# Kernel tuning notes

Hardware: AMD Instinct MI355X
Metric: run time of the kernel (lower is better)

The kernel has to match this reference:

```python
import jax, jax.numpy as jnp
import numpy as np

N = 10000      # nodes
E = 320000     # edges (before self-loops)
D_IN = 256
HID = 128
HEADS = 4
D_OUT = 256
SLOPE = 0.2    # PyG GATConv default negative_slope


def setup_inputs() -> dict:
    key = jax.random.key(0)
    ks = jax.random.split(key, 10)
    s = 0.05
    return {
        "x": jax.random.normal(ks[0], (N, D_IN), dtype=jnp.float32),
        "edge_index": jax.random.randint(ks[1], (2, E), 0, N),
        # layer 1: in=256 -> heads=4, out=128, concat
        "W1": jax.random.normal(ks[2], (D_IN, HEADS * HID), dtype=jnp.float32) * s,
        "a1_src": jax.random.normal(ks[3], (HEADS, HID), dtype=jnp.float32) * s,
        "a1_dst": jax.random.normal(ks[4], (HEADS, HID), dtype=jnp.float32) * s,
        "b1": jax.random.normal(ks[5], (HEADS * HID,), dtype=jnp.float32) * s,
        # layer 2: in=512 -> heads=1, out=256, no concat
        "W2": jax.random.normal(ks[6], (HEADS * HID, D_OUT), dtype=jnp.float32) * s,
        "a2_src": jax.random.normal(ks[7], (1, D_OUT), dtype=jnp.float32) * s,
        "a2_dst": jax.random.normal(ks[8], (1, D_OUT), dtype=jnp.float32) * s,
        "b2": jax.random.normal(ks[9], (D_OUT,), dtype=jnp.float32) * s,
    }


def gat_conv(x, src, dst, W, a_src, a_dst, bias, heads, out_dim, concat):
    """PyG-style GATConv (eval mode, self-loops pre-added to src/dst)."""
    n = x.shape[0]
    h = (x @ W).reshape(n, heads, out_dim)            # [N, H, F]
    # per-edge attention logits: LeakyReLU(a_src.h_src + a_dst.h_dst)
    as_n = (h * a_src).sum(-1)                         # [N, H]
    ad_n = (h * a_dst).sum(-1)                         # [N, H]
    logit = jax.nn.leaky_relu(as_n[src] + ad_n[dst], negative_slope=SLOPE)  # [E, H]
    # segment softmax over edges grouped by destination node
    logit = logit - jax.ops.segment_max(logit, dst, num_segments=n)[dst]
    ex = jnp.exp(logit)
    alpha = ex / jax.ops.segment_sum(ex, dst, num_segments=n)[dst]          # [E, H]
    # weighted scatter-aggregation of source messages
    out = jax.ops.segment_sum(h[src] * alpha[:, :, None], dst, num_segments=n)  # [N, H, F]
    out = out.reshape(n, heads * out_dim) if concat else out.mean(axis=1)
    return out + bias


def reference(x, edge_index, W1, a1_src, a1_dst, b1, W2, a2_src, a2_dst, b2):
    # add self-loops once (PyG GATConv default add_self_loops=True)
    loops = jnp.arange(N, dtype=edge_index.dtype)
    src = jnp.concatenate([edge_index[0], loops])
    dst = jnp.concatenate([edge_index[1], loops])
    h = gat_conv(x, src, dst, W1, a1_src, a1_dst, b1, HEADS, HID, True)
    h = jax.nn.elu(h)  # dropout is identity at eval
    return gat_conv(h, src, dst, W2, a2_src, a2_dst, b2, 1, D_OUT, False)
```

## Files before the change

kernel.cpp:

```cpp
#include <hip/hip_runtime.h>

#define N_NODES 10000
#define E_RAW   320000
#define E_TOT   330000
#define D_IN    256
#define HID     128
#define HEADS   4
#define F1      512
#define D_OUT   256
#define SLOPE   0.2f
#define EBLOCKS 1290

typedef __attribute__((ext_vector_type(8))) short bf16x8;
typedef __attribute__((ext_vector_type(4))) float f32x4;

__device__ __forceinline__ float bf2f(ushort u) {
    return __uint_as_float(((uint)u) << 16);
}
__device__ __forceinline__ ushort f2bf(float x) {
    uint u = __float_as_uint(x);
    uint r = (u + 0x7FFFu + ((u >> 16) & 1u)) >> 16;
    return (ushort)r;
}
__device__ __forceinline__ float bfu_lo(uint u) { return __uint_as_float(u << 16); }
__device__ __forceinline__ float bfu_hi(uint u) { return __uint_as_float(u & 0xFFFF0000u); }

__device__ __forceinline__ void gload_lds16(const void* g, void* l) {
    __builtin_amdgcn_global_load_lds(
        (const __attribute__((address_space(1))) void*)g,
        (__attribute__((address_space(3))) void*)l, 16, 0, 0);
}


__global__ __launch_bounds__(256) void k_zero_all(int* __restrict__ deg,
                                                  float* __restrict__ as1,
                                                  float* __restrict__ ad1,
                                                  float* __restrict__ as2,
                                                  float* __restrict__ ad2) {
    int i = blockIdx.x * 256 + threadIdx.x;
    if (i < 4 * N_NODES) { as1[i] = 0.f; ad1[i] = 0.f; }
    if (i < N_NODES) { deg[i] = 0; as2[i] = 0.f; ad2[i] = 0.f; }
}


__global__ __launch_bounds__(256) void k_hist(const int* __restrict__ ei, int* __restrict__ deg) {
    int e = blockIdx.x * 256 + threadIdx.x;
    if (e < E_TOT) {
        int dst = (e < E_RAW) ? ei[E_RAW + e] : (e - E_RAW);
        atomicAdd(&deg[dst], 1);
    }
}


#define SCAN_CHUNK 40

__global__ __launch_bounds__(256) void k_prep(const int* __restrict__ deg,
                                              int* __restrict__ row_start,
                                              int* __restrict__ cursor,
                                              const float* __restrict__ W1,
                                              ushort* __restrict__ w1h,
                                              const float* __restrict__ W2,
                                              ushort* __restrict__ w2h,
                                              const float* __restrict__ x,
                                              ushort* __restrict__ xb) {
    int b = blockIdx.x;
    int tid = threadIdx.x;
    if (b == 0) {
        __shared__ int tots[256];
        int base = tid * SCAN_CHUNK;
        int loc[SCAN_CHUNK];
        int s = 0;
        #pragma unroll
        for (int k = 0; k < SCAN_CHUNK; k++) {
            int idx = base + k;
            int v = (idx < N_NODES) ? deg[idx] : 0;
            loc[k] = s;
            s += v;
        }
        tots[tid] = s;
        __syncthreads();
        for (int off = 1; off < 256; off <<= 1) {
            int t = (tid >= off) ? tots[tid - off] : 0;
            __syncthreads();
            tots[tid] += t;
            __syncthreads();
        }
        int excl = tots[tid] - s;
        #pragma unroll
        for (int k = 0; k < SCAN_CHUNK; k++) {
            int idx = base + k;
            if (idx < N_NODES) {
                int r = excl + loc[k];
                row_start[idx] = r;
                cursor[idx]    = r;
            }
        }
        if (tid == 255) row_start[N_NODES] = E_TOT;
    } else if (b <= 512) {
        int i = (b - 1) * 256 + tid;
        int k = i / F1, n = i - k * F1;
        w1h[(size_t)n * D_IN + k] = f2bf(W1[i]);
    } else if (b <= 1024) {
        int i = (b - 513) * 256 + tid;
        int k = i / D_OUT, n = i - k * D_OUT;
        w2h[(size_t)n * F1 + k] = f2bf(W2[i]);
    } else {
        int i8 = (b - 1025) * 256 + tid;
        float4 a = *(const float4*)&x[(size_t)i8 * 8];
        float4 c = *(const float4*)&x[(size_t)i8 * 8 + 4];
        uint4 u;
        u.x = (uint)f2bf(a.x) | ((uint)f2bf(a.y) << 16);
        u.y = (uint)f2bf(a.z) | ((uint)f2bf(a.w) << 16);
        u.z = (uint)f2bf(c.x) | ((uint)f2bf(c.y) << 16);
        u.w = (uint)f2bf(c.z) | ((uint)f2bf(c.w) << 16);
        *(uint4*)&xb[(size_t)i8 * 8] = u;
    }
}


template<int BM, int KD, int ND, int WC, int HMUL>
__device__ __forceinline__ void gemm_attn(int bx, int by, int tid,
                                          const ushort* __restrict__ A,
                                          const ushort* __restrict__ B,
                                          ushort* __restrict__ C,
                                          const float* __restrict__ avs,
                                          const float* __restrict__ avd,
                                          float* __restrict__ os,
                                          float* __restrict__ od) {
    constexpr int WR = 4 / WC;
    constexpr int MI = (BM / WR) / 16;
    constexpr int NJ = (64 / WC) / 16;
    __shared__ ushort sA[BM * 64];
    __shared__ ushort sB[64 * 64];

    const int lane = tid & 63;
    const int wid = tid >> 6;
    const int wr = wid / WC;
    const int wc = wid % WC;
    const int m0 = by * BM;
    const int n0 = bx * 64;
    const int fr = lane & 15;
    const int fs = lane >> 4;
    const int rowc = lane >> 3;
    const int slot = (lane & 7) ^ rowc;

    f32x4 acc[MI][NJ];
    #pragma unroll
    for (int i = 0; i < MI; i++)
        #pragma unroll
        for (int j = 0; j < NJ; j++) acc[i][j] = (f32x4){0.f, 0.f, 0.f, 0.f};

    for (int k0 = 0; k0 < KD; k0 += 64) {
        #pragma unroll
        for (int t = 0; t < BM / 32; t++) {
            int c = wid + 4 * t;
            int gr = m0 + c * 8 + rowc;
            gr = gr < N_NODES ? gr : N_NODES - 1;
            gload_lds16(A + (size_t)gr * KD + k0 + slot * 8, &sA[c * 512]);
        }
        #pragma unroll
        for (int t = 0; t < 2; t++) {
            int c = wid + 4 * t;
            gload_lds16(B + (size_t)(n0 + c * 8 + rowc) * KD + k0 + slot * 8, &sB[c * 512]);
        }
        __syncthreads();
        #pragma unroll
        for (int kk = 0; kk < 2; kk++) {
            int sbase = kk * 4 + fs;
            bf16x8 a_f[MI], b_f[NJ];
            #pragma unroll
            for (int i = 0; i < MI; i++) {
                int r = wr * 64 + i * 16 + fr;
                a_f[i] = *(const bf16x8*)&sA[r * 64 + ((sbase ^ (r & 7)) << 3)];
            }
            #pragma unroll
            for (int j = 0; j < NJ; j++) {
                int cc = wc * (64 / WC) + j * 16 + fr;
                b_f[j] = *(const bf16x8*)&sB[cc * 64 + ((sbase ^ (cc & 7)) << 3)];
            }
            #pragma unroll
            for (int i = 0; i < MI; i++)
                #pragma unroll
                for (int j = 0; j < NJ; j++)
                    acc[i][j] = __builtin_amdgcn_mfma_f32_16x16x32_bf16(a_f[i], b_f[j], acc[i][j], 0, 0, 0);
        }
        __syncthreads();
    }

    const int hoff = (HMUL == 4) ? (n0 >> 7) : 0;
    float sv[NJ], dv[NJ];
    int cols[NJ];
    #pragma unroll
    for (int j = 0; j < NJ; j++) {
        cols[j] = n0 + wc * (64 / WC) + j * 16 + fr;
        sv[j] = avs[cols[j]];
        dv[j] = avd[cols[j]];
    }
    #pragma unroll
    for (int i = 0; i < MI; i++) {
        int row_base = m0 + wr * 64 + i * 16 + (fs << 2);
        float ps[4], pd[4];
        #pragma unroll
        for (int q = 0; q < 4; q++) {
            int r = row_base + q;
            float p_s = 0.f, p_d = 0.f;
            #pragma unroll
            for (int j = 0; j < NJ; j++) {
                float v = acc[i][j][q];
                if (r < N_NODES) C[(size_t)r * ND + cols[j]] = f2bf(v);
                p_s += v * sv[j];
                p_d += v * dv[j];
            }
            ps[q] = p_s; pd[q] = p_d;
        }
        #pragma unroll
        for (int q = 0; q < 4; q++) {
            #pragma unroll
            for (int m = 8; m >= 1; m >>= 1) {
                ps[q] += __shfl_xor(ps[q], m, 16);
                pd[q] += __shfl_xor(pd[q], m, 16);
            }
        }
        if (fr == 0) {
            #pragma unroll
            for (int q = 0; q < 4; q++) {
                int r = row_base + q;
                if (r < N_NODES) {
                    atomicAdd(&os[r * HMUL + hoff], ps[q]);
                    atomicAdd(&od[r * HMUL + hoff], pd[q]);
                }
            }
        }
    }
}


__global__ __launch_bounds__(256) void k_mid(const int* __restrict__ ei,
                                             int* __restrict__ cursor,
                                             int* __restrict__ csr_src,
                                             const ushort* __restrict__ xb,
                                             const ushort* __restrict__ w1h,
                                             ushort* __restrict__ h1,
                                             const float* __restrict__ a1s,
                                             const float* __restrict__ a1d,
                                             float* __restrict__ as1,
                                             float* __restrict__ ad1) {
    int b = blockIdx.x;
    if (b < EBLOCKS) {
        int e = b * 256 + threadIdx.x;
        if (e < E_TOT) {
            int src = (e < E_RAW) ? ei[e] : (e - E_RAW);
            int dst = (e < E_RAW) ? ei[E_RAW + e] : (e - E_RAW);
            int pos = atomicAdd(&cursor[dst], 1);
            csr_src[pos] = src;
        }
        return;
    }
    int g = b - EBLOCKS;
    gemm_attn<128, D_IN, F1, 2, 4>(g % 8, g / 8, threadIdx.x,
                                   xb, w1h, h1, a1s, a1d, as1, ad1);
}


__global__ __launch_bounds__(256) void k_gemm2(const ushort* __restrict__ heluh,
                                               const ushort* __restrict__ w2h,
                                               ushort* __restrict__ h2,
                                               const float* __restrict__ a2s,
                                               const float* __restrict__ a2d,
                                               float* __restrict__ as2,
                                               float* __restrict__ ad2) {
    int b = blockIdx.x;
    gemm_attn<64, F1, D_OUT, 4, 1>(b % 4, b / 4, threadIdx.x,
                                   heluh, w2h, h2, a2s, a2d, as2, ad2);
}


__device__ __forceinline__ void fma8(uint4 v, float e, float* acc) {
    acc[0] += bfu_lo(v.x) * e; acc[1] += bfu_hi(v.x) * e;
    acc[2] += bfu_lo(v.y) * e; acc[3] += bfu_hi(v.y) * e;
    acc[4] += bfu_lo(v.z) * e; acc[5] += bfu_hi(v.z) * e;
    acc[6] += bfu_lo(v.w) * e; acc[7] += bfu_hi(v.w) * e;
}

__global__ __launch_bounds__(256) void k_edge1(const int* __restrict__ row_start,
                                               const int* __restrict__ csr_src,
                                               const ushort* __restrict__ h1,
                                               const float* __restrict__ as1,
                                               const float* __restrict__ ad1,
                                               const float* __restrict__ b1,
                                               ushort* __restrict__ heluh) {
    int node = blockIdx.x * 4 + (threadIdx.x >> 6);
    int lane = threadIdx.x & 63;
    int start = row_start[node];
    int end   = row_start[node + 1];
    int h_lane = lane >> 4;

    float adl = ad1[node * 4 + h_lane];

    float acc[8] = {0,0,0,0,0,0,0,0};
    float sum = 0.f;
    const size_t lo8 = (size_t)lane * 8;

    int i = start;
    for (; i + 8 <= end; i += 8) {
        int s[8];
        #pragma unroll
        for (int k = 0; k < 8; k++) s[k] = csr_src[i + k];
        float l[8];
        #pragma unroll
        for (int k = 0; k < 8; k++) l[k] = as1[s[k] * 4 + h_lane];
        uint4 v[8];
        #pragma unroll
        for (int k = 0; k < 8; k++) v[k] = *(const uint4*)(h1 + (size_t)s[k] * F1 + lo8);
        #pragma unroll
        for (int k = 0; k < 8; k++) {
            float t = l[k] + adl;
            t = t > 0.f ? t : SLOPE * t;
            float e = __expf(t);
            sum += e;
            fma8(v[k], e, acc);
        }
    }
    for (; i < end; i++) {
        int s0 = csr_src[i];
        float t = as1[s0 * 4 + h_lane] + adl;
        uint4 v0 = *(const uint4*)(h1 + (size_t)s0 * F1 + lo8);
        t = t > 0.f ? t : SLOPE * t;
        float e = __expf(t);
        sum += e;
        fma8(v0, e, acc);
    }
    float inv = 1.f / sum;

    size_t o = (size_t)node * F1 + lo8;
    const float* bp = b1 + lo8;
    uint pk[4];
    #pragma unroll
    for (int j = 0; j < 4; j++) {
        float v0 = acc[2*j]   * inv + bp[2*j];
        float v1 = acc[2*j+1] * inv + bp[2*j+1];
        v0 = v0 > 0.f ? v0 : (__expf(v0) - 1.f);
        v1 = v1 > 0.f ? v1 : (__expf(v1) - 1.f);
        pk[j] = (uint)f2bf(v0) | ((uint)f2bf(v1) << 16);
    }
    *(uint4*)&heluh[o] = make_uint4(pk[0], pk[1], pk[2], pk[3]);
}

__global__ __launch_bounds__(256) void k_edge2(const int* __restrict__ row_start,
                                               const int* __restrict__ csr_src,
                                               const ushort* __restrict__ h2,
                                               const float* __restrict__ as2,
                                               const float* __restrict__ ad2,
                                               const float* __restrict__ b2,
                                               float* __restrict__ out) {
    int node = blockIdx.x * 4 + (threadIdx.x >> 6);
    int lane = threadIdx.x & 63;
    int sub = lane >> 5;
    int fl  = lane & 31;
    int start = row_start[node];
    int end   = row_start[node + 1];

    float ad = ad2[node];

    float acc[8] = {0,0,0,0,0,0,0,0};
    float sum = 0.f;
    const size_t fo = (size_t)fl * 8;

    int i = start;
    for (; i + 8 <= end; i += 8) {
        int s[4];
        #pragma unroll
        for (int k = 0; k < 4; k++) s[k] = csr_src[i + 2 * k + sub];
        float l[4];
        #pragma unroll
        for (int k = 0; k < 4; k++) l[k] = as2[s[k]];
        uint4 v[4];
        #pragma unroll
        for (int k = 0; k < 4; k++) v[k] = *(const uint4*)(h2 + (size_t)s[k] * D_OUT + fo);
        #pragma unroll
        for (int k = 0; k < 4; k++) {
            float t = l[k] + ad;
            t = t > 0.f ? t : SLOPE * t;
            float e = __expf(t);
            sum += e;
            fma8(v[k], e, acc);
        }
    }
    for (; i < end; i += 2) {
        if (i + sub < end) {
            int s0 = csr_src[i + sub];
            float t = as2[s0] + ad;
            uint4 v0 = *(const uint4*)(h2 + (size_t)s0 * D_OUT + fo);
            t = t > 0.f ? t : SLOPE * t;
            float e = __expf(t);
            sum += e;
            fma8(v0, e, acc);
        }
    }
    #pragma unroll
    for (int j = 0; j < 8; j++) acc[j] += __shfl_xor(acc[j], 32, 64);
    sum += __shfl_xor(sum, 32, 64);
    float inv = 1.f / sum;

    if (lane < 32) {
        size_t o = (size_t)node * D_OUT + fo;
        const float* bp = b2 + fo;
        float4 r0, r1;
        r0.x = acc[0] * inv + bp[0]; r0.y = acc[1] * inv + bp[1];
        r0.z = acc[2] * inv + bp[2]; r0.w = acc[3] * inv + bp[3];
        r1.x = acc[4] * inv + bp[4]; r1.y = acc[5] * inv + bp[5];
        r1.z = acc[6] * inv + bp[6]; r1.w = acc[7] * inv + bp[7];
        *(float4*)&out[o] = r0;
        *(float4*)&out[o + 4] = r1;
    }
}


extern "C" void kernel_launch(void* const* d_in, const int* in_sizes, int n_in,
                              void* d_out, int out_size, void* d_ws, size_t ws_size,
                              hipStream_t stream) {
    const float* x   = (const float*)d_in[0];
    const int*   ei  = (const int*)d_in[1];
    const float* W1  = (const float*)d_in[2];
    const float* a1s = (const float*)d_in[3];
    const float* a1d = (const float*)d_in[4];
    const float* b1  = (const float*)d_in[5];
    const float* W2  = (const float*)d_in[6];
    const float* a2s = (const float*)d_in[7];
    const float* a2d = (const float*)d_in[8];
    const float* b2  = (const float*)d_in[9];
    float* out = (float*)d_out;

    char* ws = (char*)d_ws;
    size_t off = 0;
    auto take = [&](size_t bytes) {
        char* p = ws + off;
        off += (bytes + 255) & ~(size_t)255;
        return p;
    };
    int*    deg       = (int*)take(sizeof(int) * N_NODES);
    int*    row_start = (int*)take(sizeof(int) * (N_NODES + 1));
    int*    cursor    = (int*)take(sizeof(int) * N_NODES);
    int*    csr_src   = (int*)take(sizeof(int) * E_TOT);
    ushort* xb        = (ushort*)take(sizeof(ushort) * (size_t)N_NODES * D_IN);
    ushort* w1h       = (ushort*)take(sizeof(ushort) * D_IN * F1);
    ushort* w2h       = (ushort*)take(sizeof(ushort) * F1 * D_OUT);
    ushort* h1        = (ushort*)take(sizeof(ushort) * (size_t)N_NODES * F1);
    float*  as1       = (float*)take(sizeof(float) * N_NODES * 4);
    float*  ad1       = (float*)take(sizeof(float) * N_NODES * 4);
    ushort* heluh     = (ushort*)take(sizeof(ushort) * (size_t)N_NODES * F1);
    ushort* h2        = (ushort*)take(sizeof(ushort) * (size_t)N_NODES * D_OUT);
    float*  as2       = (float*)take(sizeof(float) * N_NODES);
    float*  ad2       = (float*)take(sizeof(float) * N_NODES);

    k_zero_all<<<(4 * N_NODES + 255) / 256, 256, 0, stream>>>(deg, as1, ad1, as2, ad2);
    k_hist<<<EBLOCKS, 256, 0, stream>>>(ei, deg);
    k_prep<<<2275, 256, 0, stream>>>(deg, row_start, cursor, W1, w1h, W2, w2h, x, xb);
    k_mid<<<EBLOCKS + 8 * 79, 256, 0, stream>>>(ei, cursor, csr_src, xb, w1h, h1,
                                                a1s, a1d, as1, ad1);
    k_edge1<<<N_NODES / 4, 256, 0, stream>>>(row_start, csr_src, h1, as1, ad1, b1, heluh);
    k_gemm2<<<4 * 157, 256, 0, stream>>>(heluh, w2h, h2, a2s, a2d, as2, ad2);
    k_edge2<<<N_NODES / 4, 256, 0, stream>>>(row_start, csr_src, h2, as2, ad2, b2, out);
}
```

Measured before the change: 169.9 us.

## Double-buffer GEMM LDS tiles, vectorize weight transposes, split scatter from GEMM1

The GEMM tile loop now double-buffers its shared-memory A/B tiles, so the next K-slice load is issued before computing the current one and one barrier per iteration is dropped. The weight transpose-to-bf16 step now has each thread gather 8 K values and write them as one 16-byte store, which cuts block count and the scattered 2-byte writes. The edge CSR scatter is split out of the combined k_mid launch into its own kernel, and GEMM1 gets a dedicated kernel. This adds one kernel launch and doubles LDS use per block, which may lower occupancy.

```diff
diff --git a/kernel.cpp b/kernel.cpp
--- a/kernel.cpp
+++ b/kernel.cpp
@@ -96,16 +96,36 @@
             }
         }
         if (tid == 255) row_start[N_NODES] = E_TOT;
-    } else if (b <= 512) {
-        int i = (b - 1) * 256 + tid;
-        int k = i / F1, n = i - k * F1;
-        w1h[(size_t)n * D_IN + k] = f2bf(W1[i]);
-    } else if (b <= 1024) {
-        int i = (b - 513) * 256 + tid;
-        int k = i / D_OUT, n = i - k * D_OUT;
-        w2h[(size_t)n * F1 + k] = f2bf(W2[i]);
+    } else if (b <= 64) {
+        int task = (b - 1) * 4 + (tid >> 6);
+        int lane = tid & 63;
+        int n = (task >> 5) * 64 + lane;
+        int k0 = (task & 31) * 8;
+        float v[8];
+        #pragma unroll
+        for (int j = 0; j < 8; j++) v[j] = W1[(size_t)(k0 + j) * F1 + n];
+        uint4 u;
+        u.x = (uint)f2bf(v[0]) | ((uint)f2bf(v[1]) << 16);
+        u.y = (uint)f2bf(v[2]) | ((uint)f2bf(v[3]) << 16);
+        u.z = (uint)f2bf(v[4]) | ((uint)f2bf(v[5]) << 16);
+        u.w = (uint)f2bf(v[6]) | ((uint)f2bf(v[7]) << 16);
+        *(uint4*)&w1h[(size_t)n * D_IN + k0] = u;
+    } else if (b <= 128) {
+        int task = (b - 65) * 4 + (tid >> 6);
+        int lane = tid & 63;
+        int n = (task >> 6) * 64 + lane;
+        int k0 = (task & 63) * 8;
+        float v[8];
+        #pragma unroll
+        for (int j = 0; j < 8; j++) v[j] = W2[(size_t)(k0 + j) * D_OUT + n];
+        uint4 u;
+        u.x = (uint)f2bf(v[0]) | ((uint)f2bf(v[1]) << 16);
+        u.y = (uint)f2bf(v[2]) | ((uint)f2bf(v[3]) << 16);
+        u.z = (uint)f2bf(v[4]) | ((uint)f2bf(v[5]) << 16);
+        u.w = (uint)f2bf(v[6]) | ((uint)f2bf(v[7]) << 16);
+        *(uint4*)&w2h[(size_t)n * F1 + k0] = u;
     } else {
-        int i8 = (b - 1025) * 256 + tid;
+        int i8 = (b - 129) * 256 + tid;
         float4 a = *(const float4*)&x[(size_t)i8 * 8];
         float4 c = *(const float4*)&x[(size_t)i8 * 8 + 4];
         uint4 u;
@@ -114,6 +134,19 @@
         u.z = (uint)f2bf(c.x) | ((uint)f2bf(c.y) << 16);
         u.w = (uint)f2bf(c.z) | ((uint)f2bf(c.w) << 16);
         *(uint4*)&xb[(size_t)i8 * 8] = u;
+    }
+}
+
+
+__global__ __launch_bounds__(256) void k_scatter(const int* __restrict__ ei,
+                                                 int* __restrict__ cursor,
+                                                 int* __restrict__ csr_src) {
+    int e = blockIdx.x * 256 + threadIdx.x;
+    if (e < E_TOT) {
+        int src = (e < E_RAW) ? ei[e] : (e - E_RAW);
+        int dst = (e < E_RAW) ? ei[E_RAW + e] : (e - E_RAW);
+        int pos = atomicAdd(&cursor[dst], 1);
+        csr_src[pos] = src;
     }
 }
 
@@ -130,8 +163,9 @@
     constexpr int WR = 4 / WC;
     constexpr int MI = (BM / WR) / 16;
     constexpr int NJ = (64 / WC) / 16;
-    __shared__ ushort sA[BM * 64];
-    __shared__ ushort sB[64 * 64];
+    constexpr int NT = KD / 64;
+    __shared__ ushort sA[2][BM * 64];
+    __shared__ ushort sB[2][64 * 64];
 
     const int lane = tid & 63;
     const int wid = tid >> 6;
@@ -150,20 +184,21 @@
         #pragma unroll
         for (int j = 0; j < NJ; j++) acc[i][j] = (f32x4){0.f, 0.f, 0.f, 0.f};
 
-    for (int k0 = 0; k0 < KD; k0 += 64) {
+    auto STAGE = [&](int buf, int k0) {
         #pragma unroll
         for (int t = 0; t < BM / 32; t++) {
             int c = wid + 4 * t;
             int gr = m0 + c * 8 + rowc;
             gr = gr < N_NODES ? gr : N_NODES - 1;
-            gload_lds16(A + (size_t)gr * KD + k0 + slot * 8, &sA[c * 512]);
+            gload_lds16(A + (size_t)gr * KD + k0 + slot * 8, &sA[buf][c * 512]);
         }
         #pragma unroll
         for (int t = 0; t < 2; t++) {
             int c = wid + 4 * t;
-            gload_lds16(B + (size_t)(n0 + c * 8 + rowc) * KD + k0 + slot * 8, &sB[c * 512]);
-        }
-        __syncthreads();
+            gload_lds16(B + (size_t)(n0 + c * 8 + rowc) * KD + k0 + slot * 8, &sB[buf][c * 512]);
+        }
+    };
+    auto COMPUTE = [&](int buf) {
         #pragma unroll
         for (int kk = 0; kk < 2; kk++) {
             int sbase = kk * 4 + fs;
@@ -171,12 +206,12 @@
             #pragma unroll
             for (int i = 0; i < MI; i++) {
                 int r = wr * 64 + i * 16 + fr;
-                a_f[i] = *(const bf16x8*)&sA[r * 64 + ((sbase ^ (r & 7)) << 3)];
+                a_f[i] = *(const bf16x8*)&sA[buf][r * 64 + ((sbase ^ (r & 7)) << 3)];
             }
             #pragma unroll
             for (int j = 0; j < NJ; j++) {
                 int cc = wc * (64 / WC) + j * 16 + fr;
-                b_f[j] = *(const bf16x8*)&sB[cc * 64 + ((sbase ^ (cc & 7)) << 3)];
+                b_f[j] = *(const bf16x8*)&sB[buf][cc * 64 + ((sbase ^ (cc & 7)) << 3)];
             }
             #pragma unroll
             for (int i = 0; i < MI; i++)
@@ -184,8 +219,19 @@
                 for (int j = 0; j < NJ; j++)
                     acc[i][j] = __builtin_amdgcn_mfma_f32_16x16x32_bf16(a_f[i], b_f[j], acc[i][j], 0, 0, 0);
         }
+    };
+
+    STAGE(0, 0);
+    __syncthreads();
+    int cur = 0;
+    #pragma unroll
+    for (int t = 0; t < NT - 1; t++) {
+        STAGE(cur ^ 1, (t + 1) * 64);
+        COMPUTE(cur);
         __syncthreads();
-    }
+        cur ^= 1;
+    }
+    COMPUTE(cur);
 
     const int hoff = (HMUL == 4) ? (n0 >> 7) : 0;
     float sv[NJ], dv[NJ];
@@ -235,28 +281,14 @@
 }
 
 
-__global__ __launch_bounds__(256) void k_mid(const int* __restrict__ ei,
-                                             int* __restrict__ cursor,
-                                             int* __restrict__ csr_src,
-                                             const ushort* __restrict__ xb,
-                                             const ushort* __restrict__ w1h,
-                                             ushort* __restrict__ h1,
-                                             const float* __restrict__ a1s,
-                                             const float* __restrict__ a1d,
-                                             float* __restrict__ as1,
-                                             float* __restrict__ ad1) {
-    int b = blockIdx.x;
-    if (b < EBLOCKS) {
-        int e = b * 256 + threadIdx.x;
-        if (e < E_TOT) {
-            int src = (e < E_RAW) ? ei[e] : (e - E_RAW);
-            int dst = (e < E_RAW) ? ei[E_RAW + e] : (e - E_RAW);
-            int pos = atomicAdd(&cursor[dst], 1);
-            csr_src[pos] = src;
-        }
-        return;
-    }
-    int g = b - EBLOCKS;
+__global__ __launch_bounds__(256) void k_gemm1(const ushort* __restrict__ xb,
+                                               const ushort* __restrict__ w1h,
+                                               ushort* __restrict__ h1,
+                                               const float* __restrict__ a1s,
+                                               const float* __restrict__ a1d,
+                                               float* __restrict__ as1,
+                                               float* __restrict__ ad1) {
+    int g = blockIdx.x;
     gemm_attn<128, D_IN, F1, 2, 4>(g % 8, g / 8, threadIdx.x,
                                    xb, w1h, h1, a1s, a1d, as1, ad1);
 }
@@ -455,9 +487,9 @@
 
     k_zero_all<<<(4 * N_NODES + 255) / 256, 256, 0, stream>>>(deg, as1, ad1, as2, ad2);
     k_hist<<<EBLOCKS, 256, 0, stream>>>(ei, deg);
-    k_prep<<<2275, 256, 0, stream>>>(deg, row_start, cursor, W1, w1h, W2, w2h, x, xb);
-    k_mid<<<EBLOCKS + 8 * 79, 256, 0, stream>>>(ei, cursor, csr_src, xb, w1h, h1,
-                                                a1s, a1d, as1, ad1);
+    k_prep<<<1379, 256, 0, stream>>>(deg, row_start, cursor, W1, w1h, W2, w2h, x, xb);
+    k_scatter<<<EBLOCKS, 256, 0, stream>>>(ei, cursor, csr_src);
+    k_gemm1<<<8 * 79, 256, 0, stream>>>(xb, w1h, h1, a1s, a1d, as1, ad1);
     k_edge1<<<N_NODES / 4, 256, 0, stream>>>(row_start, csr_src, h1, as1, ad1, b1, heluh);
     k_gemm2<<<4 * 157, 256, 0, stream>>>(heluh, w2h, h2, a2s, a2d, as2, ad2);
     k_edge2<<<N_NODES / 4, 256, 0, stream>>>(row_start, csr_src, h2, as2, ad2, b2, out);
```

Measured after the change: 175.7 us. 1.03x slower.
